# Optimization experiments

Measured on AMD Instinct MI355X. Metric: run time of the kernel, lower is better.

The kernel has to match this reference:

```python
import jax, jax.numpy as jnp
import numpy as np

NEG = -1e30  # log-space 'zero'


def setup_inputs() -> dict:
    B, T, C, L = 64, 2000, 128, 200  # C = num_classes + 1, blank = C - 1
    key = jax.random.key(0)
    k1, k2, k3 = jax.random.split(key, 3)
    y_pred = jax.random.normal(k1, (B, T, C), dtype=jnp.float32)
    label_lengths = jax.random.randint(k2, (B,), L // 2, L + 1).astype(jnp.int32)
    labels = jax.random.randint(k3, (B, L), 0, C - 1).astype(jnp.int32)  # never blank
    # pad with -1 beyond each label length (matches tf sparse construction)
    valid = jnp.arange(L)[None, :] < label_lengths[:, None]
    y_true = jnp.where(valid, labels, -1).astype(jnp.int32)
    # train_step fills input_lengths with the full time dimension
    input_lengths = jnp.full((B,), T, dtype=jnp.int32)
    return {"y_pred": y_pred, "y_true": y_true,
            "input_lengths": input_lengths, "label_lengths": label_lengths}


def _lse3(a, b, c):
    m = jnp.maximum(jnp.maximum(a, b), c)
    return m + jnp.log(jnp.exp(a - m) + jnp.exp(b - m) + jnp.exp(c - m))


def _ctc_loss(y_pred, y_true, input_lengths, label_lengths):
    B, T, C = y_pred.shape
    blank = C - 1  # blank_index=-1 in tf.nn.ctc_loss
    logp = jax.nn.log_softmax(y_pred, axis=-1)          # [B,T,C]
    Lmax = y_true.shape[1]
    S = 2 * Lmax + 1                                     # extended label lattice
    lab = jnp.where(y_true < 0, 0, y_true).astype(jnp.int32)
    # extended labels: blank, l0, blank, l1, ..., blank
    ext = jnp.full((B, S), blank, jnp.int32).at[:, 1::2].set(lab)
    ext_m2 = jnp.concatenate([jnp.full((B, 2), blank, jnp.int32), ext[:, :-2]], axis=1)
    can_skip = (ext != blank) & (ext != ext_m2)          # [B,S]

    logp_t = jnp.transpose(logp, (1, 0, 2))              # [T,B,C]
    lp0 = jnp.take_along_axis(logp_t[0], ext, axis=1)    # [B,S]
    alpha = jnp.full((B, S), NEG, jnp.float32)
    alpha = alpha.at[:, 0].set(lp0[:, 0]).at[:, 1].set(lp0[:, 1])

    def step(alpha, xs):
        lp, t = xs                                       # lp: [B,C]
        lp_ext = jnp.take_along_axis(lp, ext, axis=1)    # [B,S]
        a1 = jnp.concatenate([jnp.full((B, 1), NEG, jnp.float32), alpha[:, :-1]], axis=1)
        a2 = jnp.concatenate([jnp.full((B, 2), NEG, jnp.float32), alpha[:, :-2]], axis=1)
        a2 = jnp.where(can_skip, a2, NEG)
        new = _lse3(alpha, a1, a2) + lp_ext
        new = jnp.where(t < input_lengths[:, None], new, alpha)  # freeze past seq end
        return new, None

    alpha, _ = jax.lax.scan(step, alpha, (logp_t[1:], jnp.arange(1, T)))

    s_end = (2 * label_lengths).astype(jnp.int32)        # [B]
    a_last = jnp.take_along_axis(alpha, s_end[:, None], axis=1)[:, 0]
    a_prev = jnp.take_along_axis(alpha, jnp.maximum(s_end - 1, 0)[:, None], axis=1)[:, 0]
    m = jnp.maximum(a_last, a_prev)
    ll = m + jnp.log(jnp.exp(a_last - m) + jnp.exp(a_prev - m))
    return -ll                                           # per-example loss [B]


def reference(y_pred, y_true, input_lengths, label_lengths):
    return _ctc_loss(y_pred, y_true, input_lengths, label_lengths)
```

## Files before the change

### kernel.cpp

```cpp
#include <hip/hip_runtime.h>
#include <hip/hip_fp16.h>


#define LOG2E 1.44269504088896340736f
#define LN2F  0.69314718055994530942f

namespace {

constexpr int Bc = 64, Tc = 2000, Cc = 128, Lmaxc = 200;
constexpr int ROWB = 416;
constexpr int CH = 32;
constexpr int CHB = CH * ROWB;
constexpr int BUFB = CHB + 1024;

typedef const __attribute__((address_space(1))) void* gas_ptr;
typedef __attribute__((address_space(3))) void* las_ptr;

__device__ __forceinline__ float dpp_shr1_f(float x) {
  return __int_as_float(
      __builtin_amdgcn_update_dpp(0, __float_as_int(x), 0x138, 0xF, 0xF, true));
}
__device__ __forceinline__ int dpp_shr1_i(int x) {
  return __builtin_amdgcn_update_dpp(0, x, 0x138, 0xF, 0xF, true);
}
template <int CTRL>
__device__ __forceinline__ float dpp_ctrl_add(float v) {
  return v + __int_as_float(
      __builtin_amdgcn_update_dpp(0, __float_as_int(v), CTRL, 0xF, 0xF, true));
}

__global__ __launch_bounds__(256) void pack_kernel(
    const float* __restrict__ y, const int* __restrict__ y_true,
    __half* __restrict__ W) {
  const int b = blockIdx.y;
  const int wv = threadIdx.x >> 6, lane = threadIdx.x & 63;
  const int* labs = y_true + b * Lmaxc;
  auto labc = [&](int l) -> int {
    int lc = l < 0 ? 0 : (l > Lmaxc - 1 ? Lmaxc - 1 : l);
    int c = labs[lc];
    return c < 0 ? 0 : c;
  };
  const int cA0 = labc(2 * lane), cA1 = labc(2 * lane + 1);
  const int cB0 = labc(128 + 2 * lane), cB1 = labc(129 + 2 * lane);
  const float* yb = y + (size_t)b * Tc * Cc;
  char* Wb = (char*)W + (size_t)b * Tc * ROWB;

  for (int t = blockIdx.x * 4 + wv; t < Tc; t += 64) {
    float2 yy = *(const float2*)(yb + (size_t)t * Cc + 2 * lane);
    float e0 = exp2f(fminf(yy.x * LOG2E, 50.f));
    float e1 = exp2f(fminf(yy.y * LOG2E, 50.f));
    float v = e0 + e1;
    v = dpp_ctrl_add<0x111>(v);
    v = dpp_ctrl_add<0x112>(v);
    v = dpp_ctrl_add<0x114>(v);
    v = dpp_ctrl_add<0x118>(v);
    v = dpp_ctrl_add<0x142>(v);
    v = dpp_ctrl_add<0x143>(v);
    float stot = __int_as_float(__builtin_amdgcn_readlane(__float_as_int(v), 63));
    float rs = 1.0f / stot;
    unsigned q2 = __builtin_bit_cast(unsigned, __floats2half2_rn(e0 * rs, e1 * rs));
    unsigned gA0 = (unsigned)__builtin_amdgcn_ds_bpermute((cA0 >> 1) << 2, (int)q2);
    unsigned gA1 = (unsigned)__builtin_amdgcn_ds_bpermute((cA1 >> 1) << 2, (int)q2);
    unsigned gB0 = (unsigned)__builtin_amdgcn_ds_bpermute((cB0 >> 1) << 2, (int)q2);
    unsigned gB1 = (unsigned)__builtin_amdgcn_ds_bpermute((cB1 >> 1) << 2, (int)q2);
    unsigned hA0 = (cA0 & 1) ? (gA0 >> 16) : (gA0 & 0xFFFFu);
    unsigned hA1 = (cA1 & 1) ? (gA1 >> 16) : (gA1 & 0xFFFFu);
    unsigned hB0 = (cB0 & 1) ? (gB0 >> 16) : (gB0 & 0xFFFFu);
    unsigned hB1 = (cB1 & 1) ? (gB1 >> 16) : (gB1 & 0xFFFFu);
    char* Wr = Wb + (size_t)t * ROWB;
    *(unsigned*)(Wr + 4 * lane) = hA0 | (hA1 << 16);
    if (lane < 38) *(unsigned*)(Wr + 256 + 4 * lane) = hB0 | (hB1 << 16);
    if (lane == 0) {
      unsigned bl = (unsigned)__builtin_amdgcn_readlane((int)q2, 63) >> 16;
      *(unsigned short*)(Wr + 408) = (unsigned short)bl;
      *(unsigned short*)(Wr + 410) = 0;
      *(unsigned*)(Wr + 412) = 0;
    }
  }
}

__global__ __launch_bounds__(64) void ctc_alpha_kernel(
    const __half* __restrict__ W, const int* __restrict__ y_true,
    const int* __restrict__ in_len, const int* __restrict__ lab_len,
    float* __restrict__ out) {
  __shared__ __align__(16) char buf[2][BUFB];
  const int b = blockIdx.x, lane = threadIdx.x;
  int len = in_len[b];
  len = len < 1 ? 1 : (len > Tc ? Tc : len);
  const int ll = lab_len[b];
  const int* labs = y_true + b * Lmaxc;
  auto labc = [&](int l) -> int {
    int lc = l < 0 ? 0 : (l > Lmaxc - 1 ? Lmaxc - 1 : l);
    int c = labs[lc];
    return c < 0 ? 0 : c;
  };
  const int c0i = labc(4 * lane), c1i = labc(4 * lane + 1);
  const int c2i = labc(4 * lane + 2), c3i = labc(4 * lane + 3);
  const int cm1 = labc(4 * lane - 1), cm2 = labc(4 * lane - 2);
  const float sk0 = (4 * lane >= 1 && c0i != cm1) ? 1.f : 0.f;
  const float sk1 = (c1i != c0i) ? 1.f : 0.f;
  const float sk2 = (c2i != c1i) ? 1.f : 0.f;
  const float sk3 = (c3i != c2i) ? 1.f : 0.f;
  const float skH = (lane >= 1 && cm1 != cm2) ? 1.f : 0.f;
  const int lane8 = 8 * lane;

  const char* Wb = (const char*)W + (size_t)b * Tc * ROWB;
  const unsigned maxoff = (unsigned)Tc * ROWB - 16;
  auto load_chunk = [&](int bufi, int k) {
#pragma unroll
    for (int j = 0; j < 14; ++j) {
      unsigned off = (unsigned)(1 + CH * k) * ROWB + j * 1024 + lane * 16;
      off = off > maxoff ? maxoff : off;
      __builtin_amdgcn_global_load_lds((gas_ptr)(Wb + off),
                                       (las_ptr)(&buf[bufi][j * 1024]), 16, 0, 0);
    }
  };
  auto rd = [&](const char* base, int row, uint2& lab, unsigned short& bl) {
    const char* r = base + row * ROWB;
    lab = *(const uint2*)(r + lane8);
    bl = *(const unsigned short*)(r + 408);
  };

  float a0 = 0.f, a1 = 0.f, a2 = 0.f, a3 = 0.f;
  float a4 = 0.f, a5 = 0.f, a6 = 0.f, a7 = 0.f;
  int E = 0;
  {
    float l0 = __half2float(*(const __half*)(Wb + 0));
    float b0 = __half2float(*(const __half*)(Wb + 408));
    if (lane == 0) { a0 = b0; a1 = l0; }
  }
  float s7d = dpp_shr1_f(a7), s6d = dpp_shr1_f(a6), s5d = dpp_shr1_f(a5);
  int epd = 0;
  float corr = (lane == 0) ? 0.f : 1.f;

  const int NR = len - 1;
  const int NCg = (NR + CH - 1) / CH;
  const int cfull = NR / CH;
  if (NCg > 0) load_chunk(0, 0);

  for (int c = 0; c < cfull; ++c) {
    __syncthreads();
    if (c + 1 < NCg) load_chunk((c + 1) & 1, c + 1);
    const char* base = buf[c & 1];
    uint2 labA[3], labB[3];
    unsigned short blA[3], blB[3];
    rd(base, 0, labA[0], blA[0]);
    rd(base, 1, labB[0], blB[0]);
    rd(base, 2, labA[1], blA[1]);
    rd(base, 3, labB[1], blB[1]);
#pragma unroll
    for (int rr = 0; rr < 16; ++rr) {
      const int p = rr % 3, pf = (rr + 2) % 3;
      if (rr < 14) {
        rd(base, 2 * rr + 4, labA[pf], blA[pf]);
        rd(base, 2 * rr + 5, labB[pf], blB[pf]);
      }
      const float2 aLo = __half22float2(*(__half2*)&labA[p].x);
      const float2 aHi = __half22float2(*(__half2*)&labA[p].y);
      const float2 bLo = __half22float2(*(__half2*)&labB[p].x);
      const float2 bHi = __half22float2(*(__half2*)&labB[p].y);
      const float qbA = __half2float(*(__half*)&blA[p]);
      const float qbB = __half2float(*(__half*)&blB[p]);
      const float qhA = dpp_shr1_f(aHi.y);
      const float w7 = s7d * corr, w6 = s6d * corr, w5 = s5d * corr;
      const float hA = (w7 + w6 + skH * w5) * qhA;
      float n0 = (a0 + w7) * qbA;
      float n1 = (a1 + a0 + sk0 * w7) * aLo.x;
      float n2 = (a2 + a1) * qbA;
      float n3 = (a3 + a2 + sk1 * a1) * aLo.y;
      float n4 = (a4 + a3) * qbA;
      float n5 = (a5 + a4 + sk2 * a3) * aHi.x;
      float n6 = (a6 + a5) * qbA;
      float n7 = (a7 + a6 + sk3 * a5) * aHi.y;
      a0 = (n0 + hA) * qbB;
      a1 = (n1 + n0 + sk0 * hA) * bLo.x;
      a2 = (n2 + n1) * qbB;
      a3 = (n3 + n2 + sk1 * n1) * bLo.y;
      a4 = (n4 + n3) * qbB;
      a5 = (n5 + n4 + sk2 * n3) * bHi.x;
      a6 = (n6 + n5) * qbB;
      a7 = (n7 + n6 + sk3 * n5) * bHi.y;
      if ((rr & 3) == 3) {
        float mx = fmaxf(fmaxf(fmaxf(a0, a1), fmaxf(a2, a3)),
                         fmaxf(fmaxf(a4, a5), fmaxf(a6, a7)));
        unsigned bits = __float_as_uint(mx);
        bool z = (bits == 0u);
        int e = (int)(bits >> 23) - 127;
        float f = __uint_as_float((254u - (bits >> 23)) << 23);
        f = z ? 1.0f : f;
        a0 *= f; a1 *= f; a2 *= f; a3 *= f;
        a4 *= f; a5 *= f; a6 *= f; a7 *= f;
        E = z ? epd : (E + e);
      }
      s7d = dpp_shr1_f(a7);
      s6d = dpp_shr1_f(a6);
      s5d = dpp_shr1_f(a5);
      if ((rr & 3) == 3) {
        epd = dpp_shr1_i(E);
        int de = epd - E;
        de = de < -126 ? -126 : (de > 60 ? 60 : de);
        corr = __int_as_float((de + 127) << 23);
        corr = (lane == 0) ? 0.0f : corr;
      }
    }
  }

  const int rem = NR - cfull * CH;
  if (rem > 0) {
    __syncthreads();
    const char* base = buf[cfull & 1];
    for (int r = 0; r < rem; ++r) {
      const char* rp = base + r * ROWB;
      uint2 lab = *(const uint2*)(rp + lane8);
      float2 flo = __half22float2(*(__half2*)&lab.x);
      float2 fhi = __half22float2(*(__half2*)&lab.y);
      float bl = __half2float(*(const __half*)(rp + 408));
      float s7 = dpp_shr1_f(a7);
      int ep = dpp_shr1_i(E);
      int de = ep - E;
      de = de < -126 ? -126 : (de > 60 ? 60 : de);
      float c2 = __int_as_float((de + 127) << 23);
      c2 = (lane == 0) ? 0.0f : c2;
      float w7 = s7 * c2;
      float n0 = (a0 + w7) * bl;
      float n1 = (a1 + a0 + sk0 * w7) * flo.x;
      float n2 = (a2 + a1) * bl;
      float n3 = (a3 + a2 + sk1 * a1) * flo.y;
      float n4 = (a4 + a3) * bl;
      float n5 = (a5 + a4 + sk2 * a3) * fhi.x;
      float n6 = (a6 + a5) * bl;
      float n7 = (a7 + a6 + sk3 * a5) * fhi.y;
      a0 = n0; a1 = n1; a2 = n2; a3 = n3;
      a4 = n4; a5 = n5; a6 = n6; a7 = n7;
      if ((r & 3) == 3) {
        float mx = fmaxf(fmaxf(fmaxf(a0, a1), fmaxf(a2, a3)),
                         fmaxf(fmaxf(a4, a5), fmaxf(a6, a7)));
        unsigned bits = __float_as_uint(mx);
        bool z = (bits == 0u);
        int e = (int)(bits >> 23) - 127;
        float f = __uint_as_float((254u - (bits >> 23)) << 23);
        f = z ? 1.0f : f;
        a0 *= f; a1 *= f; a2 *= f; a3 *= f;
        a4 *= f; a5 *= f; a6 *= f; a7 *= f;
        E = z ? ep : (E + e);
      }
    }
  }

  int sE = 2 * ll;
  int sP = sE - 1 < 0 ? 0 : sE - 1;
  int laneA = sE >> 3, jA = sE & 7;
  int laneB = sP >> 3, jB = sP & 7;
  float va = a0;
  if (jA == 1) va = a1;
  if (jA == 2) va = a2;
  if (jA == 3) va = a3;
  if (jA == 4) va = a4;
  if (jA == 5) va = a5;
  if (jA == 6) va = a6;
  if (jA == 7) va = a7;
  float vb = a0;
  if (jB == 1) vb = a1;
  if (jB == 2) vb = a2;
  if (jB == 3) vb = a3;
  if (jB == 4) vb = a4;
  if (jB == 5) vb = a5;
  if (jB == 6) vb = a6;
  if (jB == 7) vb = a7;
  float aA = __int_as_float(__builtin_amdgcn_ds_bpermute(laneA << 2, __float_as_int(va)));
  float aB = __int_as_float(__builtin_amdgcn_ds_bpermute(laneB << 2, __float_as_int(vb)));
  int EA = __builtin_amdgcn_ds_bpermute(laneA << 2, E);
  int EB = __builtin_amdgcn_ds_bpermute(laneB << 2, E);
  if (lane == 0) {
    float l1 = (aA > 0.0f) ? (float)EA + log2f(aA) : -1e30f;
    float l2 = (aB > 0.0f) ? (float)EB + log2f(aB) : -1e30f;
    float mm = fmaxf(l1, l2);
    float v = mm + log2f(exp2f(l1 - mm) + exp2f(l2 - mm));
    out[b] = -v * LN2F;
  }
}

}

extern "C" void kernel_launch(void* const* d_in, const int* in_sizes, int n_in,
                              void* d_out, int out_size, void* d_ws, size_t ws_size,
                              hipStream_t stream) {
  const float* y = (const float*)d_in[0];
  const int* yt = (const int*)d_in[1];
  const int* il = (const int*)d_in[2];
  const int* lb = (const int*)d_in[3];
  float* out = (float*)d_out;
  __half* W = (__half*)d_ws;

  hipLaunchKernelGGL(pack_kernel, dim3(16, 64), dim3(256), 0, stream, y, yt, W);
  hipLaunchKernelGGL(ctc_alpha_kernel, dim3(Bc), dim3(64), 0, stream,
                     W, yt, il, lb, out);
}
```

Measured before the change: 268.8 us.

## Repack emissions into per-lane paired-timestep layout with blank array and deeper prefetch

```diff
diff --git a/kernel.cpp b/kernel.cpp
--- a/kernel.cpp
+++ b/kernel.cpp
@@ -8,10 +8,12 @@
 namespace {
 
 constexpr int Bc = 64, Tc = 2000, Cc = 128, Lmaxc = 200;
-constexpr int ROWB = 416;
-constexpr int CH = 32;
-constexpr int CHB = CH * ROWB;
-constexpr int BUFB = CHB + 1024;
+constexpr int NPAIR = Tc / 2;
+constexpr int PAIRB = 1024;
+constexpr int BLANKB = 8192;
+constexpr size_t SB = (size_t)NPAIR * PAIRB + BLANKB;
+constexpr int CHP = 16;
+constexpr int CHB = CHP * PAIRB;
 
 typedef const __attribute__((address_space(1))) void* gas_ptr;
 typedef __attribute__((address_space(3))) void* las_ptr;
@@ -24,66 +26,65 @@
   return __builtin_amdgcn_update_dpp(0, x, 0x138, 0xF, 0xF, true);
 }
 template <int CTRL>
-__device__ __forceinline__ float dpp_ctrl_add(float v) {
+__device__ __forceinline__ float dpp_add(float v) {
   return v + __int_as_float(
       __builtin_amdgcn_update_dpp(0, __float_as_int(v), CTRL, 0xF, 0xF, true));
 }
+__device__ __forceinline__ float wave_sum_bcast(float v) {
+  v = dpp_add<0x111>(v);
+  v = dpp_add<0x112>(v);
+  v = dpp_add<0x114>(v);
+  v = dpp_add<0x118>(v);
+  v = dpp_add<0x142>(v);
+  v = dpp_add<0x143>(v);
+  return __int_as_float(__builtin_amdgcn_readlane(__float_as_int(v), 63));
+}
 
 __global__ __launch_bounds__(256) void pack_kernel(
     const float* __restrict__ y, const int* __restrict__ y_true,
-    __half* __restrict__ W) {
+    char* __restrict__ W) {
   const int b = blockIdx.y;
   const int wv = threadIdx.x >> 6, lane = threadIdx.x & 63;
+  const int t = blockIdx.x * 4 + wv;
   const int* labs = y_true + b * Lmaxc;
-  auto labc = [&](int l) -> int {
-    int lc = l < 0 ? 0 : (l > Lmaxc - 1 ? Lmaxc - 1 : l);
-    int c = labs[lc];
-    return c < 0 ? 0 : c;
-  };
-  const int cA0 = labc(2 * lane), cA1 = labc(2 * lane + 1);
-  const int cB0 = labc(128 + 2 * lane), cB1 = labc(129 + 2 * lane);
-  const float* yb = y + (size_t)b * Tc * Cc;
-  char* Wb = (char*)W + (size_t)b * Tc * ROWB;
-
-  for (int t = blockIdx.x * 4 + wv; t < Tc; t += 64) {
-    float2 yy = *(const float2*)(yb + (size_t)t * Cc + 2 * lane);
-    float e0 = exp2f(fminf(yy.x * LOG2E, 50.f));
-    float e1 = exp2f(fminf(yy.y * LOG2E, 50.f));
-    float v = e0 + e1;
-    v = dpp_ctrl_add<0x111>(v);
-    v = dpp_ctrl_add<0x112>(v);
-    v = dpp_ctrl_add<0x114>(v);
-    v = dpp_ctrl_add<0x118>(v);
-    v = dpp_ctrl_add<0x142>(v);
-    v = dpp_ctrl_add<0x143>(v);
-    float stot = __int_as_float(__builtin_amdgcn_readlane(__float_as_int(v), 63));
-    float rs = 1.0f / stot;
-    unsigned q2 = __builtin_bit_cast(unsigned, __floats2half2_rn(e0 * rs, e1 * rs));
-    unsigned gA0 = (unsigned)__builtin_amdgcn_ds_bpermute((cA0 >> 1) << 2, (int)q2);
-    unsigned gA1 = (unsigned)__builtin_amdgcn_ds_bpermute((cA1 >> 1) << 2, (int)q2);
-    unsigned gB0 = (unsigned)__builtin_amdgcn_ds_bpermute((cB0 >> 1) << 2, (int)q2);
-    unsigned gB1 = (unsigned)__builtin_amdgcn_ds_bpermute((cB1 >> 1) << 2, (int)q2);
-    unsigned hA0 = (cA0 & 1) ? (gA0 >> 16) : (gA0 & 0xFFFFu);
-    unsigned hA1 = (cA1 & 1) ? (gA1 >> 16) : (gA1 & 0xFFFFu);
-    unsigned hB0 = (cB0 & 1) ? (gB0 >> 16) : (gB0 & 0xFFFFu);
-    unsigned hB1 = (cB1 & 1) ? (gB1 >> 16) : (gB1 & 0xFFFFu);
-    char* Wr = Wb + (size_t)t * ROWB;
-    *(unsigned*)(Wr + 4 * lane) = hA0 | (hA1 << 16);
-    if (lane < 38) *(unsigned*)(Wr + 256 + 4 * lane) = hB0 | (hB1 << 16);
-    if (lane == 0) {
-      unsigned bl = (unsigned)__builtin_amdgcn_readlane((int)q2, 63) >> 16;
-      *(unsigned short*)(Wr + 408) = (unsigned short)bl;
-      *(unsigned short*)(Wr + 410) = 0;
-      *(unsigned*)(Wr + 412) = 0;
-    }
+  int base = 4 * lane;
+  if (base > Lmaxc - 4) base = Lmaxc - 4;
+  const int4 L = *(const int4*)(labs + base);
+  auto fix = [&](int v, int idx) {
+    int r = (idx > Lmaxc - 1) ? L.w : v;
+    return r < 0 ? 0 : r;
+  };
+  const int c0 = fix(L.x, 4 * lane), c1 = fix(L.y, 4 * lane + 1);
+  const int c2 = fix(L.z, 4 * lane + 2), c3 = fix(L.w, 4 * lane + 3);
+  const float2 yy = *(const float2*)(y + ((size_t)b * Tc + t) * Cc + 2 * lane);
+  float e0 = exp2f(fminf(yy.x * LOG2E, 50.f));
+  float e1 = exp2f(fminf(yy.y * LOG2E, 50.f));
+  const float rs = 1.0f / wave_sum_bcast(e0 + e1);
+  unsigned q2 = __builtin_bit_cast(unsigned, __floats2half2_rn(e0 * rs, e1 * rs));
+  unsigned g0 = (unsigned)__builtin_amdgcn_ds_bpermute((c0 >> 1) << 2, (int)q2);
+  unsigned g1 = (unsigned)__builtin_amdgcn_ds_bpermute((c1 >> 1) << 2, (int)q2);
+  unsigned g2 = (unsigned)__builtin_amdgcn_ds_bpermute((c2 >> 1) << 2, (int)q2);
+  unsigned g3 = (unsigned)__builtin_amdgcn_ds_bpermute((c3 >> 1) << 2, (int)q2);
+  unsigned h0 = (c0 & 1) ? (g0 >> 16) : (g0 & 0xFFFFu);
+  unsigned h1 = (c1 & 1) ? (g1 >> 16) : (g1 & 0xFFFFu);
+  unsigned h2 = (c2 & 1) ? (g2 >> 16) : (g2 & 0xFFFFu);
+  unsigned h3 = (c3 & 1) ? (g3 >> 16) : (g3 & 0xFFFFu);
+  if (t > 0) {
+    char* Wb = W + (size_t)b * SB;
+    const int pr = (t - 1) >> 1, sl = 1 - (t & 1);
+    *(uint2*)(Wb + pr * PAIRB + lane * 16 + sl * 8) =
+        make_uint2(h0 | (h1 << 16), h2 | (h3 << 16));
+    if (lane == 63)
+      *(float*)(Wb + (size_t)NPAIR * PAIRB + (size_t)(t - 1) * 4) = e1 * rs;
   }
 }
 
 __global__ __launch_bounds__(64) void ctc_alpha_kernel(
-    const __half* __restrict__ W, const int* __restrict__ y_true,
-    const int* __restrict__ in_len, const int* __restrict__ lab_len,
-    float* __restrict__ out) {
-  __shared__ __align__(16) char buf[2][BUFB];
+    const float* __restrict__ y, const char* __restrict__ W,
+    const int* __restrict__ y_true, const int* __restrict__ in_len,
+    const int* __restrict__ lab_len, float* __restrict__ out) {
+  __shared__ __align__(16) char bufs[2][CHB];
+  __shared__ __align__(16) float blk_s[BLANKB / 4];
   const int b = blockIdx.x, lane = threadIdx.x;
   int len = in_len[b];
   len = len < 1 ? 1 : (len > Tc ? Tc : len);
@@ -102,119 +103,150 @@
   const float sk2 = (c2i != c1i) ? 1.f : 0.f;
   const float sk3 = (c3i != c2i) ? 1.f : 0.f;
   const float skH = (lane >= 1 && cm1 != cm2) ? 1.f : 0.f;
-  const int lane8 = 8 * lane;
-
-  const char* Wb = (const char*)W + (size_t)b * Tc * ROWB;
-  const unsigned maxoff = (unsigned)Tc * ROWB - 16;
-  auto load_chunk = [&](int bufi, int k) {
+  const int lane16 = lane * 16;
+
+  const char* Wb = W + (size_t)b * SB;
+  auto load_pairs = [&](int bi, int k) {
 #pragma unroll
-    for (int j = 0; j < 14; ++j) {
-      unsigned off = (unsigned)(1 + CH * k) * ROWB + j * 1024 + lane * 16;
-      off = off > maxoff ? maxoff : off;
+    for (int j = 0; j < CHP; ++j) {
+      unsigned off = (unsigned)(CHP * k + j) * PAIRB + lane16;
       __builtin_amdgcn_global_load_lds((gas_ptr)(Wb + off),
-                                       (las_ptr)(&buf[bufi][j * 1024]), 16, 0, 0);
-    }
-  };
-  auto rd = [&](const char* base, int row, uint2& lab, unsigned short& bl) {
-    const char* r = base + row * ROWB;
-    lab = *(const uint2*)(r + lane8);
-    bl = *(const unsigned short*)(r + 408);
+                                       (las_ptr)(&bufs[bi][j * PAIRB]), 16, 0, 0);
+    }
+  };
+  auto load_blanks = [&]() {
+#pragma unroll
+    for (int j = 0; j < 8; ++j)
+      __builtin_amdgcn_global_load_lds(
+          (gas_ptr)(Wb + NPAIR * PAIRB + j * 1024 + lane16),
+          (las_ptr)((char*)blk_s + j * 1024), 16, 0, 0);
   };
 
   float a0 = 0.f, a1 = 0.f, a2 = 0.f, a3 = 0.f;
   float a4 = 0.f, a5 = 0.f, a6 = 0.f, a7 = 0.f;
   int E = 0;
   {
-    float l0 = __half2float(*(const __half*)(Wb + 0));
-    float b0 = __half2float(*(const __half*)(Wb + 408));
-    if (lane == 0) { a0 = b0; a1 = l0; }
+    const float* y0 = y + (size_t)b * Tc * Cc + 2 * lane;
+    float e0 = exp2f(fminf(y0[0] * LOG2E, 50.f));
+    float e1 = exp2f(fminf(y0[1] * LOG2E, 50.f));
+    const float rs = 1.0f / wave_sum_bcast(e0 + e1);
+    int l0 = labs[0];
+    l0 = l0 < 0 ? 0 : l0;
+    float ev = (l0 & 1) ? e1 : e0;
+    float q0 = __int_as_float(__builtin_amdgcn_readlane(__float_as_int(ev), l0 >> 1)) * rs;
+    float qb = __int_as_float(__builtin_amdgcn_readlane(__float_as_int(e1), 63)) * rs;
+    if (lane == 0) { a0 = qb; a1 = q0; }
   }
   float s7d = dpp_shr1_f(a7), s6d = dpp_shr1_f(a6), s5d = dpp_shr1_f(a5);
   int epd = 0;
   float corr = (lane == 0) ? 0.f : 1.f;
 
-  const int NR = len - 1;
-  const int NCg = (NR + CH - 1) / CH;
-  const int cfull = NR / CH;
-  if (NCg > 0) load_chunk(0, 0);
+  auto round2 = [&](uint4 rw, float2 bl, bool renorm) {
+    float2 aLo = __half22float2(*(__half2*)&rw.x);
+    float2 aHi = __half22float2(*(__half2*)&rw.y);
+    float2 bLo = __half22float2(*(__half2*)&rw.z);
+    float2 bHi = __half22float2(*(__half2*)&rw.w);
+    const float qbA = bl.x, qbB = bl.y;
+    const float qhA = dpp_shr1_f(aHi.y);
+    const float w7 = s7d * corr, w6 = s6d * corr, w5 = s5d * corr;
+    const float hA = (w7 + w6 + skH * w5) * qhA;
+    float n0 = (a0 + w7) * qbA;
+    float n1 = (a1 + a0 + sk0 * w7) * aLo.x;
+    float n2 = (a2 + a1) * qbA;
+    float n3 = (a3 + a2 + sk1 * a1) * aLo.y;
+    float n4 = (a4 + a3) * qbA;
+    float n5 = (a5 + a4 + sk2 * a3) * aHi.x;
+    float n6 = (a6 + a5) * qbA;
+    float n7 = (a7 + a6 + sk3 * a5) * aHi.y;
+    a0 = (n0 + hA) * qbB;
+    a1 = (n1 + n0 + sk0 * hA) * bLo.x;
+    a2 = (n2 + n1) * qbB;
+    a3 = (n3 + n2 + sk1 * n1) * bLo.y;
+    a4 = (n4 + n3) * qbB;
+    a5 = (n5 + n4 + sk2 * n3) * bHi.x;
+    a6 = (n6 + n5) * qbB;
+    a7 = (n7 + n6 + sk3 * n5) * bHi.y;
+    if (renorm) {
+      float mx = fmaxf(fmaxf(fmaxf(a0, a1), fmaxf(a2, a3)),
+                       fmaxf(fmaxf(a4, a5), fmaxf(a6, a7)));
+      unsigned bits = __float_as_uint(mx);
+      bool z = (bits == 0u);
+      int e = (int)(bits >> 23) - 127;
+      float f = __uint_as_float((254u - (bits >> 23)) << 23);
+      f = z ? 1.0f : f;
+      a0 *= f; a1 *= f; a2 *= f; a3 *= f;
+      a4 *= f; a5 *= f; a6 *= f; a7 *= f;
+      E = z ? epd : (E + e);
+    }
+    s7d = dpp_shr1_f(a7);
+    s6d = dpp_shr1_f(a6);
+    s5d = dpp_shr1_f(a5);
+    if (renorm) {
+      epd = dpp_shr1_i(E);
+      int de = epd - E;
+      de = de < -126 ? -126 : (de > 60 ? 60 : de);
+      corr = __int_as_float((de + 127) << 23);
+      corr = (lane == 0) ? 0.0f : corr;
+    }
+  };
+
+  const int R = (len - 1) >> 1;
+  const int leftover = (len - 1) & 1;
+  const int PRtot = R + leftover;
+  const int NCg = (PRtot + CHP - 1) / CHP;
+  const int cfull = R / CHP;
+
+  load_blanks();
+  if (NCg > 0) load_pairs(0, 0);
+  __builtin_amdgcn_s_waitcnt(0x0f70);
+  if (NCg > 1) load_pairs(1, 1);
+
+  uint4 raw[2];
+  float2 blkp[2];
+  if (NCg > 0) {
+    raw[0] = *(const uint4*)(&bufs[0][0 * PAIRB] + lane16);
+    blkp[0] = *(const float2*)(blk_s + 0);
+    raw[1] = *(const uint4*)(&bufs[0][1 * PAIRB] + lane16);
+    blkp[1] = *(const float2*)(blk_s + 2);
+  }
 
   for (int c = 0; c < cfull; ++c) {
-    __syncthreads();
-    if (c + 1 < NCg) load_chunk((c + 1) & 1, c + 1);
-    const char* base = buf[c & 1];
-    uint2 labA[3], labB[3];
-    unsigned short blA[3], blB[3];
-    rd(base, 0, labA[0], blA[0]);
-    rd(base, 1, labB[0], blB[0]);
-    rd(base, 2, labA[1], blA[1]);
-    rd(base, 3, labB[1], blB[1]);
+    const char* base = &bufs[c & 1][0];
+    const char* nbase = &bufs[(c + 1) & 1][0];
+    const float* pb = blk_s + c * 32;
 #pragma unroll
     for (int rr = 0; rr < 16; ++rr) {
-      const int p = rr % 3, pf = (rr + 2) % 3;
+      const int p = rr & 1;
+      uint4 rw = raw[p];
+      float2 bl = blkp[p];
       if (rr < 14) {
-        rd(base, 2 * rr + 4, labA[pf], blA[pf]);
-        rd(base, 2 * rr + 5, labB[pf], blB[pf]);
+        raw[p] = *(const uint4*)(base + (rr + 2) * PAIRB + lane16);
+        blkp[p] = *(const float2*)(pb + (rr + 2) * 2);
+      } else {
+        if (rr == 14) __builtin_amdgcn_s_waitcnt(0x0f70);
+        raw[p] = *(const uint4*)(nbase + (rr - 14) * PAIRB + lane16);
+        blkp[p] = *(const float2*)(pb + 32 + (rr - 14) * 2);
       }
-      const float2 aLo = __half22float2(*(__half2*)&labA[p].x);
-      const float2 aHi = __half22float2(*(__half2*)&labA[p].y);
-      const float2 bLo = __half22float2(*(__half2*)&labB[p].x);
-      const float2 bHi = __half22float2(*(__half2*)&labB[p].y);
-      const float qbA = __half2float(*(__half*)&blA[p]);
-      const float qbB = __half2float(*(__half*)&blB[p]);
-      const float qhA = dpp_shr1_f(aHi.y);
-      const float w7 = s7d * corr, w6 = s6d * corr, w5 = s5d * corr;
-      const float hA = (w7 + w6 + skH * w5) * qhA;
-      float n0 = (a0 + w7) * qbA;
-      float n1 = (a1 + a0 + sk0 * w7) * aLo.x;
-      float n2 = (a2 + a1) * qbA;
-      float n3 = (a3 + a2 + sk1 * a1) * aLo.y;
-      float n4 = (a4 + a3) * qbA;
-      float n5 = (a5 + a4 + sk2 * a3) * aHi.x;
-      float n6 = (a6 + a5) * qbA;
-      float n7 = (a7 + a6 + sk3 * a5) * aHi.y;
-      a0 = (n0 + hA) * qbB;
-      a1 = (n1 + n0 + sk0 * hA) * bLo.x;
-      a2 = (n2 + n1) * qbB;
-      a3 = (n3 + n2 + sk1 * n1) * bLo.y;
-      a4 = (n4 + n3) * qbB;
-      a5 = (n5 + n4 + sk2 * n3) * bHi.x;
-      a6 = (n6 + n5) * qbB;
-      a7 = (n7 + n6 + sk3 * n5) * bHi.y;
-      if ((rr & 3) == 3) {
-        float mx = fmaxf(fmaxf(fmaxf(a0, a1), fmaxf(a2, a3)),
-                         fmaxf(fmaxf(a4, a5), fmaxf(a6, a7)));
-        unsigned bits = __float_as_uint(mx);
-        bool z = (bits == 0u);
-        int e = (int)(bits >> 23) - 127;
-        float f = __uint_as_float((254u - (bits >> 23)) << 23);
-        f = z ? 1.0f : f;
-        a0 *= f; a1 *= f; a2 *= f; a3 *= f;
-        a4 *= f; a5 *= f; a6 *= f; a7 *= f;
-        E = z ? epd : (E + e);
-      }
-      s7d = dpp_shr1_f(a7);
-      s6d = dpp_shr1_f(a6);
-      s5d = dpp_shr1_f(a5);
-      if ((rr & 3) == 3) {
-        epd = dpp_shr1_i(E);
-        int de = epd - E;
-        de = de < -126 ? -126 : (de > 60 ? 60 : de);
-        corr = __int_as_float((de + 127) << 23);
-        corr = (lane == 0) ? 0.0f : corr;
-      }
-    }
-  }
-
-  const int rem = NR - cfull * CH;
-  if (rem > 0) {
-    __syncthreads();
-    const char* base = buf[cfull & 1];
+      round2(rw, bl, (rr & 3) == 3);
+    }
+    if (c + 2 < NCg) load_pairs(c & 1, c + 2);
+  }
+
+  __builtin_amdgcn_s_waitcnt(0x0f70);
+  {
+    const char* tb = &bufs[cfull & 1][0];
+    const float* pbT = blk_s + cfull * 32;
+    const int rem = R - cfull * CHP;
     for (int r = 0; r < rem; ++r) {
-      const char* rp = base + r * ROWB;
-      uint2 lab = *(const uint2*)(rp + lane8);
-      float2 flo = __half22float2(*(__half2*)&lab.x);
-      float2 fhi = __half22float2(*(__half2*)&lab.y);
-      float bl = __half2float(*(const __half*)(rp + 408));
+      uint4 rw = *(const uint4*)(tb + r * PAIRB + lane16);
+      float2 bl = *(const float2*)(pbT + 2 * r);
+      round2(rw, bl, (r & 3) == 3);
+    }
+    if (leftover) {
+      uint4 rw = *(const uint4*)(tb + rem * PAIRB + lane16);
+      float blA = *(pbT + 2 * rem);
+      float2 flo = __half22float2(*(__half2*)&rw.x);
+      float2 fhi = __half22float2(*(__half2*)&rw.y);
       float s7 = dpp_shr1_f(a7);
       int ep = dpp_shr1_i(E);
       int de = ep - E;
@@ -222,28 +254,16 @@
       float c2 = __int_as_float((de + 127) << 23);
       c2 = (lane == 0) ? 0.0f : c2;
       float w7 = s7 * c2;
-      float n0 = (a0 + w7) * bl;
+      float n0 = (a0 + w7) * blA;
       float n1 = (a1 + a0 + sk0 * w7) * flo.x;
-      float n2 = (a2 + a1) * bl;
+      float n2 = (a2 + a1) * blA;
       float n3 = (a3 + a2 + sk1 * a1) * flo.y;
-      float n4 = (a4 + a3) * bl;
+      float n4 = (a4 + a3) * blA;
       float n5 = (a5 + a4 + sk2 * a3) * fhi.x;
-      float n6 = (a6 + a5) * bl;
+      float n6 = (a6 + a5) * blA;
       float n7 = (a7 + a6 + sk3 * a5) * fhi.y;
       a0 = n0; a1 = n1; a2 = n2; a3 = n3;
       a4 = n4; a5 = n5; a6 = n6; a7 = n7;
-      if ((r & 3) == 3) {
-        float mx = fmaxf(fmaxf(fmaxf(a0, a1), fmaxf(a2, a3)),
-                         fmaxf(fmaxf(a4, a5), fmaxf(a6, a7)));
-        unsigned bits = __float_as_uint(mx);
-        bool z = (bits == 0u);
-        int e = (int)(bits >> 23) - 127;
-        float f = __uint_as_float((254u - (bits >> 23)) << 23);
-        f = z ? 1.0f : f;
-        a0 *= f; a1 *= f; a2 *= f; a3 *= f;
-        a4 *= f; a5 *= f; a6 *= f; a7 *= f;
-        E = z ? ep : (E + e);
-      }
     }
   }
 
@@ -290,9 +310,9 @@
   const int* il = (const int*)d_in[2];
   const int* lb = (const int*)d_in[3];
   float* out = (float*)d_out;
-  __half* W = (__half*)d_ws;
-
-  hipLaunchKernelGGL(pack_kernel, dim3(16, 64), dim3(256), 0, stream, y, yt, W);
+  char* W = (char*)d_ws;
+
+  hipLaunchKernelGGL(pack_kernel, dim3(Tc / 4, Bc), dim3(256), 0, stream, y, yt, W);
   hipLaunchKernelGGL(ctc_alpha_kernel, dim3(Bc), dim3(64), 0, stream,
-                     W, yt, il, lb, out);
-}
+                     y, W, yt, il, lb, out);
+}
```

Measured after the change: 258.9 us. 3.7% less time.
